# Performance work log

Measured on AMD Instinct MI355X. Metric: run time of the kernel, lower is better.

## Reference

```python
import jax, jax.numpy as jnp
import numpy as np

G = 8  # order of C8 rotation group

def expand_circulant(w):
    # w: [out_fields, in_fields, G] free params of a C8 regular->regular 1x1 conv.
    # Full weight: W[of*G+go, if*G+gi] = w[of, if, (go-gi) mod G]
    g = jnp.arange(G)
    idx = (g[:, None] - g[None, :]) % G            # [go, gi]
    Wf = w[:, :, idx]                              # [of, if, go, gi]
    Wf = jnp.transpose(Wf, (0, 2, 1, 3))           # [of, go, if, gi]
    return Wf.reshape(w.shape[0] * G, w.shape[1] * G)

def eq_proj(x2, w, b):
    # x2: [B, in_fields*G]; equivariant 1x1 conv = GEMM with circulant-expanded weight
    Wf = expand_circulant(w)                       # [out_fields*G, in_fields*G]
    bf = jnp.repeat(b, G)                          # per-field bias, shared across group dim
    return x2 @ Wf.T + bf

def setup_inputs() -> dict:
    key = jax.random.key(0)
    ks = jax.random.split(key, 12)
    B, d_model, n_head, d_k, d_v = 8192, 128, 8, 64, 64
    C = d_model * G                                # 1024
    s_in = 0.02
    inp = {
        'q': jax.random.normal(ks[0], (B, C, 1, 1), jnp.float32),
        'k': jax.random.normal(ks[1], (B, C, 1, 1), jnp.float32),
        'v': jax.random.normal(ks[2], (B, C, 1, 1), jnp.float32),
        'w_q': jax.random.normal(ks[3], (n_head * d_k, d_model, G), jnp.float32) * s_in,
        'b_q': jnp.zeros((n_head * d_k,), jnp.float32),
        'w_k': jax.random.normal(ks[4], (n_head * d_k, d_model, G), jnp.float32) * s_in,
        'b_k': jnp.zeros((n_head * d_k,), jnp.float32),
        'w_v': jax.random.normal(ks[5], (n_head * d_v, d_model, G), jnp.float32) * s_in,
        'b_v': jnp.zeros((n_head * d_v,), jnp.float32),
        'w_fc': jax.random.normal(ks[6], (d_model, n_head * d_v, G), jnp.float32) * s_in,
        'b_fc': jnp.zeros((d_model,), jnp.float32),
    }
    return inp

def reference(q, k, v, w_q, b_q, w_k, b_k, w_v, b_v, w_fc, b_fc):
    B, C = q.shape[0], q.shape[1]
    n_head, d_k = 8, 64
    d_v = 64
    temp = jnp.asarray(d_k ** 0.5, q.dtype)
    residual = q                                   # [B, C, 1, 1]
    q2 = q.reshape(B, C)
    k2 = k.reshape(B, C)
    v2 = v.reshape(B, C)
    # equivariant 1x1 conv projections -> [B, n_head*d_k*G]
    qp = eq_proj(q2, w_q, b_q).reshape(B, G, n_head, d_k).transpose(0, 2, 1, 3)  # [B,H,G,dk]
    kp = eq_proj(k2, w_k, b_k).reshape(B, G, n_head, d_k).transpose(0, 2, 1, 3)
    vp = eq_proj(v2, w_v, b_v).reshape(B, G, n_head, d_v).transpose(0, 2, 1, 3)
    # scaled dot-product attention over the G=8 group/orientation positions
    attn = jax.nn.softmax(jnp.einsum('bhqd,bhkd->bhqk', qp / temp, kp), axis=-1)  # [B,H,G,G]
    out = jnp.einsum('bhqk,bhkd->bhqd', attn, vp)  # [B,H,G,dv]
    # transpose(1,2) then flatten, exactly as torch .view(sz_b, -1, 1, 1)
    out = out.transpose(0, 2, 1, 3).reshape(B, G * n_head * d_v)
    out = eq_proj(out, w_fc, b_fc)                 # [B, d_model*G]
    out = out.reshape(B, C, 1, 1) + residual
    return out, attn
```

## Files before the change

### kernel.cpp

```cpp
#include <hip/hip_runtime.h>
#include <hip/hip_bf16.h>

typedef unsigned short u16;
typedef unsigned int u32;
typedef __bf16 bf16x8_t __attribute__((ext_vector_type(8)));
typedef float f32x4_t __attribute__((ext_vector_type(4)));

#define TILE 128
#define BK 64

__device__ __forceinline__ float b2f(u16 v) {
  return __uint_as_float(((u32)v) << 16);
}
__device__ __forceinline__ u16 f2b(float f) {
  __hip_bfloat16 h = __float2bfloat16(f);
  return *reinterpret_cast<u16*>(&h);
}
__device__ __forceinline__ float blo(u32 u) { return __uint_as_float(u << 16); }
__device__ __forceinline__ float bhi(u32 u) { return __uint_as_float(u & 0xffff0000u); }

__device__ __forceinline__ void async_lds16(const u16* g, u16* l) {
  __builtin_amdgcn_global_load_lds(
      (__attribute__((address_space(1))) void*)g,
      (__attribute__((address_space(3))) void*)l, 16, 0, 0);
}

__device__ __forceinline__ void cvt8(const float* __restrict__ src,
                                     u16* __restrict__ dst, size_t i) {
  float4 a = *(const float4*)(src + i);
  float4 b = *(const float4*)(src + i + 4);
  u16 t[8] = {f2b(a.x), f2b(a.y), f2b(a.z), f2b(a.w),
              f2b(b.x), f2b(b.y), f2b(b.z), f2b(b.w)};
  *(uint4*)(dst + i) = *(const uint4*)t;
}

__device__ __forceinline__ void expand8(const float* __restrict__ w,
                                        u16* __restrict__ dst, int I,
                                        int kshift, int gid) {
  const int n = gid >> kshift;
  const int kc = (gid & ((1 << kshift) - 1)) * 8;
  const int K = 8 << kshift;
  const float* wp = w + (size_t)((n >> 3) * I + (kc >> 3)) * 8;
  float4 w0 = *(const float4*)wp;
  float4 w1 = *(const float4*)(wp + 4);
  float w8[8] = {w0.x, w0.y, w0.z, w0.w, w1.x, w1.y, w1.z, w1.w};
  u16 t[8];
  const int r = (n - kc) & 7;
#pragma unroll
  for (int j = 0; j < 8; ++j) t[j] = f2b(w8[(r - j) & 7]);
  *(uint4*)(dst + (size_t)n * K + kc) = *(const uint4*)t;
}

__global__ __launch_bounds__(256) void prep_kernel(
    const float* __restrict__ q, const float* __restrict__ k,
    const float* __restrict__ v, u16* __restrict__ qb, u16* __restrict__ kb,
    u16* __restrict__ vb, const float* __restrict__ w_q,
    const float* __restrict__ w_k, const float* __restrict__ w_v,
    const float* __restrict__ w_fc, u16* __restrict__ Wq, u16* __restrict__ Wk,
    u16* __restrict__ Wv, u16* __restrict__ Wfc, int C) {
  const int bid = blockIdx.x;
  const int tid = threadIdx.x;
  if (bid < 3 * C) {
    const int plane = bid / C;
    const int b2 = bid - plane * C;
    const float* src = (plane == 0) ? q : (plane == 1) ? k : v;
    u16* dst = (plane == 0) ? qb : (plane == 1) ? kb : vb;
    cvt8(src, dst, ((size_t)b2 * 256 + tid) * 8);
  } else {
    const int e = bid - 3 * C;
    const int plane = e >> 11;
    const int gid = (e & 2047) * 256 + tid;
    if (plane == 0) expand8(w_q, Wq, 128, 7, gid);
    else if (plane == 1) expand8(w_k, Wk, 128, 7, gid);
    else if (plane == 2) expand8(w_v, Wv, 128, 7, gid);
    else expand8(w_fc, Wfc, 512, 9, gid);
  }
}

template <bool HAS_RES, bool OUT_F32>
__device__ __forceinline__ void gemm_core(
    const u16* __restrict__ X, const u16* __restrict__ W,
    const float* __restrict__ bias, const float* __restrict__ res,
    void* __restrict__ Yv, int M, int N, int K, int bid) {
  __shared__ __align__(16) u16 As[TILE * BK];
  __shared__ __align__(16) u16 Bs[TILE * BK];
  const int tid = threadIdx.x;

  const int grid_m = M >> 7, grid_n = N >> 7;
  const int nb = grid_m * grid_n;
  int pid = (bid & 7) * (nb >> 3) + (bid >> 3);
  const int nig = 8 * grid_n;
  const int group_id = pid / nig;
  const int first_m = group_id * 8;
  const int gsz = min(8, grid_m - first_m);
  const int mt = first_m + (pid % gsz);
  const int nt = (pid % nig) / gsz;
  const int m0 = mt << 7, n0 = nt << 7;

  const int lane = tid & 63;
  const int wave = tid >> 6;
  const int wm = (wave >> 1) * 64;
  const int wn = (wave & 1) * 64;
  const int l16 = lane & 15;
  const int quad = lane >> 4;

  f32x4_t acc[4][4] = {};

  const int row0 = tid >> 3;
  const int kgl = ((tid & 7) ^ (row0 & 7)) * 8;

  for (int k0 = 0; k0 < K; k0 += BK) {
#pragma unroll
    for (int it = 0; it < 4; ++it) {
      const int row = row0 + it * 32;
      const int off = (tid + it * 256) * 8;
      async_lds16(X + (size_t)(m0 + row) * K + (k0 + kgl), &As[off]);
      async_lds16(W + (size_t)(n0 + row) * K + (k0 + kgl), &Bs[off]);
    }
    __syncthreads();
#pragma unroll
    for (int half = 0; half < 2; ++half) {
      bf16x8_t af[4], bfr[4];
#pragma unroll
      for (int i = 0; i < 4; ++i)
        af[i] = *(const bf16x8_t*)&As[(wm + i * 16 + l16) * BK +
                                      (((quad + half * 4) ^ (l16 & 7)) * 8)];
#pragma unroll
      for (int j = 0; j < 4; ++j)
        bfr[j] = *(const bf16x8_t*)&Bs[(wn + j * 16 + l16) * BK +
                                       (((quad + half * 4) ^ (l16 & 7)) * 8)];
#pragma unroll
      for (int i = 0; i < 4; ++i)
#pragma unroll
        for (int j = 0; j < 4; ++j)
          acc[i][j] =
              __builtin_amdgcn_mfma_f32_16x16x32_bf16(af[i], bfr[j], acc[i][j], 0, 0, 0);
    }
    __syncthreads();
  }

#pragma unroll
  for (int j = 0; j < 4; ++j) {
    const int col = n0 + wn + j * 16 + l16;
    const float bv = bias[col >> 3];
#pragma unroll
    for (int i = 0; i < 4; ++i) {
#pragma unroll
      for (int r = 0; r < 4; ++r) {
        const int rw = m0 + wm + i * 16 + quad * 4 + r;
        float vv = acc[i][j][r] + bv;
        if (HAS_RES) vv += res[(size_t)rw * N + col];
        if (OUT_F32)
          ((float*)Yv)[(size_t)rw * N + col] = vv;
        else
          ((u16*)Yv)[(size_t)rw * N + col] = f2b(vv);
      }
    }
  }
}

__global__ __launch_bounds__(256) void gemm_qkv(
    const u16* __restrict__ X0, const u16* __restrict__ X1,
    const u16* __restrict__ X2, const u16* __restrict__ W0,
    const u16* __restrict__ W1, const u16* __restrict__ W2,
    const float* __restrict__ b0, const float* __restrict__ b1,
    const float* __restrict__ b2, u16* __restrict__ Y0, u16* __restrict__ Y1,
    u16* __restrict__ Y2, int M, int N, int K) {
  const int z = blockIdx.y;
  const u16* X = (z == 0) ? X0 : (z == 1) ? X1 : X2;
  const u16* W = (z == 0) ? W0 : (z == 1) ? W1 : W2;
  const float* bb = (z == 0) ? b0 : (z == 1) ? b1 : b2;
  u16* Y = (z == 0) ? Y0 : (z == 1) ? Y1 : Y2;
  gemm_core<false, false>(X, W, bb, nullptr, Y, M, N, K, blockIdx.x);
}

__global__ __launch_bounds__(256) void gemm_fc(
    const u16* __restrict__ X, const u16* __restrict__ W,
    const float* __restrict__ bias, const float* __restrict__ res,
    float* __restrict__ Y, int M, int N, int K) {
  gemm_core<true, true>(X, W, bias, res, Y, M, N, K, blockIdx.x);
}

__global__ __launch_bounds__(256) void attn_kernel(
    const u16* __restrict__ qp, const u16* __restrict__ kp,
    const u16* __restrict__ vp, float* __restrict__ probs,
    u16* __restrict__ o, int iters) {
  __shared__ __align__(16) u16 Qs[4][8 * 72];
  __shared__ __align__(16) u16 Ks[4][8 * 72];
  __shared__ __align__(16) u16 Vs[4][8 * 72];
  __shared__ float Ps[4][64];
  const int tid = threadIdx.x;
  const int wave = tid >> 6;
  const int lane = tid & 63;
  const int r = lane >> 3, c = lane & 7;
  const int ls = r * 72 + c * 8;
  const int qg = lane >> 3;
  const int kg = lane & 7;

  auto gaddr = [&](int it) {
    const int pair = (it * gridDim.x + blockIdx.x) * 4 + wave;
    return (size_t)(pair >> 3) * 4096 + (size_t)r * 512 + (pair & 7) * 64 + c * 8;
  };

  uint4 qr = *(const uint4*)(qp + gaddr(0));
  uint4 kr = *(const uint4*)(kp + gaddr(0));
  uint4 vr = *(const uint4*)(vp + gaddr(0));

  for (int it = 0; it < iters; ++it) {
    *(uint4*)&Qs[wave][ls] = qr;
    *(uint4*)&Ks[wave][ls] = kr;
    *(uint4*)&Vs[wave][ls] = vr;
    if (it + 1 < iters) {
      qr = *(const uint4*)(qp + gaddr(it + 1));
      kr = *(const uint4*)(kp + gaddr(it + 1));
      vr = *(const uint4*)(vp + gaddr(it + 1));
    }
    const int pair = (it * gridDim.x + blockIdx.x) * 4 + wave;
    const int b = pair >> 3;
    const int h = pair & 7;
    float s = 0.f;
#pragma unroll
    for (int d8 = 0; d8 < 8; ++d8) {
      uint4 qa = *(const uint4*)&Qs[wave][qg * 72 + d8 * 8];
      uint4 ka = *(const uint4*)&Ks[wave][kg * 72 + d8 * 8];
      s += blo(qa.x) * blo(ka.x) + bhi(qa.x) * bhi(ka.x);
      s += blo(qa.y) * blo(ka.y) + bhi(qa.y) * bhi(ka.y);
      s += blo(qa.z) * blo(ka.z) + bhi(qa.z) * bhi(ka.z);
      s += blo(qa.w) * blo(ka.w) + bhi(qa.w) * bhi(ka.w);
    }
    s *= 0.125f;
    float mx = s;
    mx = fmaxf(mx, __shfl_xor(mx, 1));
    mx = fmaxf(mx, __shfl_xor(mx, 2));
    mx = fmaxf(mx, __shfl_xor(mx, 4));
    float e = __expf(s - mx);
    float sum = e;
    sum += __shfl_xor(sum, 1);
    sum += __shfl_xor(sum, 2);
    sum += __shfl_xor(sum, 4);
    const float p = e / sum;
    probs[(size_t)pair * 64 + lane] = p;
    Ps[wave][lane] = p;
    float vc[8];
#pragma unroll
    for (int k2 = 0; k2 < 8; ++k2) vc[k2] = b2f(Vs[wave][k2 * 72 + lane]);
#pragma unroll
    for (int q2 = 0; q2 < 8; ++q2) {
      float acc = 0.f;
#pragma unroll
      for (int k2 = 0; k2 < 8; ++k2) acc += Ps[wave][q2 * 8 + k2] * vc[k2];
      o[(size_t)b * 4096 + q2 * 512 + h * 64 + lane] = f2b(acc);
    }
  }
}

extern "C" void kernel_launch(void* const* d_in, const int* in_sizes, int n_in,
                              void* d_out, int out_size, void* d_ws, size_t ws_size,
                              hipStream_t stream) {
  const float* q = (const float*)d_in[0];
  const float* k = (const float*)d_in[1];
  const float* v = (const float*)d_in[2];
  const float* w_q = (const float*)d_in[3];
  const float* b_q = (const float*)d_in[4];
  const float* w_k = (const float*)d_in[5];
  const float* b_k = (const float*)d_in[6];
  const float* w_v = (const float*)d_in[7];
  const float* b_v = (const float*)d_in[8];
  const float* w_fc = (const float*)d_in[9];
  const float* b_fc = (const float*)d_in[10];

  const int B = in_sizes[0] / 1024;
  float* out = (float*)d_out;
  float* probs = out + (size_t)B * 1024;

  u16* Wq = (u16*)d_ws;
  u16* Wk = Wq + (size_t)4096 * 1024;
  u16* Wv = Wk + (size_t)4096 * 1024;
  u16* Wfc = Wv + (size_t)4096 * 1024;
  u16* scratch = Wfc + (size_t)4096 * 1024;
  const size_t wbytes = (size_t)4 * 4096 * 1024 * sizeof(u16);

  const size_t per_row = (size_t)(3 * 1024 + 4 * 4096) * sizeof(u16);
  int chunkB = 128;
  for (int c = B; c >= 128; c >>= 1) {
    if (wbytes + (size_t)c * per_row <= ws_size) { chunkB = c; break; }
  }

  u16* qb = scratch;
  u16* kb = qb + (size_t)chunkB * 1024;
  u16* vb = kb + (size_t)chunkB * 1024;
  u16* qp = vb + (size_t)chunkB * 1024;
  u16* kp = qp + (size_t)chunkB * 4096;
  u16* vp = kp + (size_t)chunkB * 4096;
  u16* ao = vp + (size_t)chunkB * 4096;

  for (int cs = 0; cs < B; cs += chunkB) {
    const int C = chunkB / 2;
    const int prepBlocks = 3 * C + (cs == 0 ? 4 * 2048 : 0);
    prep_kernel<<<prepBlocks, 256, 0, stream>>>(
        q + (size_t)cs * 1024, k + (size_t)cs * 1024, v + (size_t)cs * 1024,
        qb, kb, vb, w_q, w_k, w_v, w_fc, Wq, Wk, Wv, Wfc, C);

    const int nb_p = (chunkB / TILE) * (4096 / TILE);
    gemm_qkv<<<dim3(nb_p, 3), 256, 0, stream>>>(qb, kb, vb, Wq, Wk, Wv, b_q,
                                                b_k, b_v, qp, kp, vp, chunkB,
                                                4096, 1024);
    const int ablocks = (chunkB >= 1024) ? 2048 : chunkB * 2;
    const int aiters = (chunkB * 8) / (ablocks * 4);
    attn_kernel<<<ablocks, 256, 0, stream>>>(qp, kp, vp,
                                             probs + (size_t)cs * 512, ao, aiters);
    const int nb_fc = (chunkB / TILE) * (1024 / TILE);
    gemm_fc<<<nb_fc, 256, 0, stream>>>(ao, Wfc, b_fc, q + (size_t)cs * 1024,
                                       out + (size_t)cs * 1024, chunkB, 1024,
                                       4096);
  }
}
```

Before: 658.9 us.

## Fuse fp32-to-bf16 input conversion into QKV GEMM and narrow FC tile

Drops the separate prep pass that wrote bf16 copies of q/k/v. The QKV GEMM now loads fp32 activations directly, converts them in registers and stores them to LDS, which removes a full extra read/write pass and the scratch buffers it used. Weight expansion moves to its own kernel, launched once. The FC GEMM uses 64-wide N tiles to get more blocks, and the attention kernel reads V straight from global instead of staging it in LDS. In exchange, A-tile loads become synchronous register loads rather than async LDS loads, which may expose more latency in the QKV GEMM.

```diff
diff --git a/kernel.cpp b/kernel.cpp
--- a/kernel.cpp
+++ b/kernel.cpp
@@ -6,7 +6,6 @@
 typedef __bf16 bf16x8_t __attribute__((ext_vector_type(8)));
 typedef float f32x4_t __attribute__((ext_vector_type(4)));
 
-#define TILE 128
 #define BK 64
 
 __device__ __forceinline__ float b2f(u16 v) {
@@ -23,15 +22,6 @@
   __builtin_amdgcn_global_load_lds(
       (__attribute__((address_space(1))) void*)g,
       (__attribute__((address_space(3))) void*)l, 16, 0, 0);
-}
-
-__device__ __forceinline__ void cvt8(const float* __restrict__ src,
-                                     u16* __restrict__ dst, size_t i) {
-  float4 a = *(const float4*)(src + i);
-  float4 b = *(const float4*)(src + i + 4);
-  u16 t[8] = {f2b(a.x), f2b(a.y), f2b(a.z), f2b(a.w),
-              f2b(b.x), f2b(b.y), f2b(b.z), f2b(b.w)};
-  *(uint4*)(dst + i) = *(const uint4*)t;
 }
 
 __device__ __forceinline__ void expand8(const float* __restrict__ w,
@@ -51,42 +41,30 @@
   *(uint4*)(dst + (size_t)n * K + kc) = *(const uint4*)t;
 }
 
-__global__ __launch_bounds__(256) void prep_kernel(
-    const float* __restrict__ q, const float* __restrict__ k,
-    const float* __restrict__ v, u16* __restrict__ qb, u16* __restrict__ kb,
-    u16* __restrict__ vb, const float* __restrict__ w_q,
-    const float* __restrict__ w_k, const float* __restrict__ w_v,
-    const float* __restrict__ w_fc, u16* __restrict__ Wq, u16* __restrict__ Wk,
-    u16* __restrict__ Wv, u16* __restrict__ Wfc, int C) {
-  const int bid = blockIdx.x;
-  const int tid = threadIdx.x;
-  if (bid < 3 * C) {
-    const int plane = bid / C;
-    const int b2 = bid - plane * C;
-    const float* src = (plane == 0) ? q : (plane == 1) ? k : v;
-    u16* dst = (plane == 0) ? qb : (plane == 1) ? kb : vb;
-    cvt8(src, dst, ((size_t)b2 * 256 + tid) * 8);
-  } else {
-    const int e = bid - 3 * C;
-    const int plane = e >> 11;
-    const int gid = (e & 2047) * 256 + tid;
-    if (plane == 0) expand8(w_q, Wq, 128, 7, gid);
-    else if (plane == 1) expand8(w_k, Wk, 128, 7, gid);
-    else if (plane == 2) expand8(w_v, Wv, 128, 7, gid);
-    else expand8(w_fc, Wfc, 512, 9, gid);
-  }
-}
-
-template <bool HAS_RES, bool OUT_F32>
+__global__ __launch_bounds__(256) void expand_all(
+    const float* __restrict__ w_q, const float* __restrict__ w_k,
+    const float* __restrict__ w_v, const float* __restrict__ w_fc,
+    u16* __restrict__ Wq, u16* __restrict__ Wk, u16* __restrict__ Wv,
+    u16* __restrict__ Wfc) {
+  const int e = blockIdx.x;
+  const int plane = e >> 11;
+  const int gid = (e & 2047) * 256 + threadIdx.x;
+  if (plane == 0) expand8(w_q, Wq, 128, 7, gid);
+  else if (plane == 1) expand8(w_k, Wk, 128, 7, gid);
+  else if (plane == 2) expand8(w_v, Wv, 128, 7, gid);
+  else expand8(w_fc, Wfc, 512, 9, gid);
+}
+
+template <int TN, bool HAS_RES, bool OUT_F32, bool A_F32>
 __device__ __forceinline__ void gemm_core(
-    const u16* __restrict__ X, const u16* __restrict__ W,
+    const void* __restrict__ Xv, const u16* __restrict__ W,
     const float* __restrict__ bias, const float* __restrict__ res,
     void* __restrict__ Yv, int M, int N, int K, int bid) {
-  __shared__ __align__(16) u16 As[TILE * BK];
-  __shared__ __align__(16) u16 Bs[TILE * BK];
+  __shared__ __align__(16) u16 As[128 * BK];
+  __shared__ __align__(16) u16 Bs[TN * BK];
   const int tid = threadIdx.x;
 
-  const int grid_m = M >> 7, grid_n = N >> 7;
+  const int grid_m = M >> 7, grid_n = N / TN;
   const int nb = grid_m * grid_n;
   int pid = (bid & 7) * (nb >> 3) + (bid >> 3);
   const int nig = 8 * grid_n;
@@ -95,44 +73,64 @@
   const int gsz = min(8, grid_m - first_m);
   const int mt = first_m + (pid % gsz);
   const int nt = (pid % nig) / gsz;
-  const int m0 = mt << 7, n0 = nt << 7;
+  const int m0 = mt << 7, n0 = nt * TN;
 
   const int lane = tid & 63;
   const int wave = tid >> 6;
   const int wm = (wave >> 1) * 64;
-  const int wn = (wave & 1) * 64;
+  const int wn = (wave & 1) * (TN / 2);
   const int l16 = lane & 15;
   const int quad = lane >> 4;
-
-  f32x4_t acc[4][4] = {};
+  constexpr int NJ = TN >> 5;
+
+  f32x4_t acc[4][NJ] = {};
 
   const int row0 = tid >> 3;
   const int kgl = ((tid & 7) ^ (row0 & 7)) * 8;
 
   for (int k0 = 0; k0 < K; k0 += BK) {
 #pragma unroll
-    for (int it = 0; it < 4; ++it) {
-      const int row = row0 + it * 32;
-      const int off = (tid + it * 256) * 8;
-      async_lds16(X + (size_t)(m0 + row) * K + (k0 + kgl), &As[off]);
-      async_lds16(W + (size_t)(n0 + row) * K + (k0 + kgl), &Bs[off]);
+    for (int it = 0; it < TN / 32; ++it)
+      async_lds16(W + (size_t)(n0 + row0 + it * 32) * K + (k0 + kgl),
+                  &Bs[(tid + it * 256) * 8]);
+    if (A_F32) {
+      const float* Xf = (const float*)Xv;
+      float4 fa[4], fb[4];
+#pragma unroll
+      for (int it = 0; it < 4; ++it) {
+        const float* p = Xf + (size_t)(m0 + row0 + it * 32) * K + (k0 + kgl);
+        fa[it] = *(const float4*)p;
+        fb[it] = *(const float4*)(p + 4);
+      }
+#pragma unroll
+      for (int it = 0; it < 4; ++it) {
+        u16 t[8] = {f2b(fa[it].x), f2b(fa[it].y), f2b(fa[it].z), f2b(fa[it].w),
+                    f2b(fb[it].x), f2b(fb[it].y), f2b(fb[it].z), f2b(fb[it].w)};
+        *(uint4*)&As[(tid + it * 256) * 8] = *(const uint4*)t;
+      }
+    } else {
+      const u16* Xb = (const u16*)Xv;
+#pragma unroll
+      for (int it = 0; it < 4; ++it)
+        async_lds16(Xb + (size_t)(m0 + row0 + it * 32) * K + (k0 + kgl),
+                    &As[(tid + it * 256) * 8]);
     }
     __syncthreads();
 #pragma unroll
     for (int half = 0; half < 2; ++half) {
-      bf16x8_t af[4], bfr[4];
+      bf16x8_t af[4], bfr[NJ];
 #pragma unroll
       for (int i = 0; i < 4; ++i)
         af[i] = *(const bf16x8_t*)&As[(wm + i * 16 + l16) * BK +
                                       (((quad + half * 4) ^ (l16 & 7)) * 8)];
 #pragma unroll
-      for (int j = 0; j < 4; ++j)
+      for (int j = 0; j < NJ; ++j)
         bfr[j] = *(const bf16x8_t*)&Bs[(wn + j * 16 + l16) * BK +
                                        (((quad + half * 4) ^ (l16 & 7)) * 8)];
 #pragma unroll
       for (int i = 0; i < 4; ++i)
 #pragma unroll
-        for (int j = 0; j < 4; ++j)
+        for (int j = 0; j < NJ; ++j)
           acc[i][j] =
               __builtin_amdgcn_mfma_f32_16x16x32_bf16(af[i], bfr[j], acc[i][j], 0, 0, 0);
     }
@@ -140,7 +138,7 @@
   }
 
 #pragma unroll
-  for (int j = 0; j < 4; ++j) {
+  for (int j = 0; j < NJ; ++j) {
     const int col = n0 + wn + j * 16 + l16;
     const float bv = bias[col >> 3];
 #pragma unroll
@@ -160,25 +158,25 @@
 }
 
 __global__ __launch_bounds__(256) void gemm_qkv(
-    const u16* __restrict__ X0, const u16* __restrict__ X1,
-    const u16* __restrict__ X2, const u16* __restrict__ W0,
+    const float* __restrict__ X0, const float* __restrict__ X1,
+    const float* __restrict__ X2, const u16* __restrict__ W0,
     const u16* __restrict__ W1, const u16* __restrict__ W2,
     const float* __restrict__ b0, const float* __restrict__ b1,
     const float* __restrict__ b2, u16* __restrict__ Y0, u16* __restrict__ Y1,
     u16* __restrict__ Y2, int M, int N, int K) {
   const int z = blockIdx.y;
-  const u16* X = (z == 0) ? X0 : (z == 1) ? X1 : X2;
+  const float* X = (z == 0) ? X0 : (z == 1) ? X1 : X2;
   const u16* W = (z == 0) ? W0 : (z == 1) ? W1 : W2;
   const float* bb = (z == 0) ? b0 : (z == 1) ? b1 : b2;
   u16* Y = (z == 0) ? Y0 : (z == 1) ? Y1 : Y2;
-  gemm_core<false, false>(X, W, bb, nullptr, Y, M, N, K, blockIdx.x);
+  gemm_core<128, false, false, true>(X, W, bb, nullptr, Y, M, N, K, blockIdx.x);
 }
 
 __global__ __launch_bounds__(256) void gemm_fc(
     const u16* __restrict__ X, const u16* __restrict__ W,
     const float* __restrict__ bias, const float* __restrict__ res,
     float* __restrict__ Y, int M, int N, int K) {
-  gemm_core<true, true>(X, W, bias, res, Y, M, N, K, blockIdx.x);
+  gemm_core<64, true, true, false>(X, W, bias, res, Y, M, N, K, blockIdx.x);
 }
 
 __global__ __launch_bounds__(256) void attn_kernel(
@@ -187,37 +185,38 @@
     u16* __restrict__ o, int iters) {
   __shared__ __align__(16) u16 Qs[4][8 * 72];
   __shared__ __align__(16) u16 Ks[4][8 * 72];
-  __shared__ __align__(16) u16 Vs[4][8 * 72];
-  __shared__ float Ps[4][64];
+  __shared__ __align__(16) float Ps[4][64];
   const int tid = threadIdx.x;
   const int wave = tid >> 6;
   const int lane = tid & 63;
   const int r = lane >> 3, c = lane & 7;
   const int ls = r * 72 + c * 8;
-  const int qg = lane >> 3;
-  const int kg = lane & 7;
-
+  const int qg = r;
+  const int kg = c;
+
+  auto pairof = [&](int it) { return (it * gridDim.x + blockIdx.x) * 4 + wave; };
   auto gaddr = [&](int it) {
-    const int pair = (it * gridDim.x + blockIdx.x) * 4 + wave;
-    return (size_t)(pair >> 3) * 4096 + (size_t)r * 512 + (pair & 7) * 64 + c * 8;
+    const int pr = pairof(it);
+    return (size_t)(pr >> 3) * 4096 + (size_t)r * 512 + (pr & 7) * 64 + c * 8;
   };
 
   uint4 qr = *(const uint4*)(qp + gaddr(0));
   uint4 kr = *(const uint4*)(kp + gaddr(0));
-  uint4 vr = *(const uint4*)(vp + gaddr(0));
 
   for (int it = 0; it < iters; ++it) {
     *(uint4*)&Qs[wave][ls] = qr;
     *(uint4*)&Ks[wave][ls] = kr;
-    *(uint4*)&Vs[wave][ls] = vr;
+    const int pair = pairof(it);
+    const int b = pair >> 3;
+    const int h = pair & 7;
+    float vcf[8];
+#pragma unroll
+    for (int k2 = 0; k2 < 8; ++k2)
+      vcf[k2] = b2f(vp[(size_t)b * 4096 + (size_t)k2 * 512 + h * 64 + lane]);
     if (it + 1 < iters) {
       qr = *(const uint4*)(qp + gaddr(it + 1));
       kr = *(const uint4*)(kp + gaddr(it + 1));
-      vr = *(const uint4*)(vp + gaddr(it + 1));
-    }
-    const int pair = (it * gridDim.x + blockIdx.x) * 4 + wave;
-    const int b = pair >> 3;
-    const int h = pair & 7;
+    }
     float s = 0.f;
 #pragma unroll
     for (int d8 = 0; d8 < 8; ++d8) {
@@ -241,14 +240,12 @@
     const float p = e / sum;
     probs[(size_t)pair * 64 + lane] = p;
     Ps[wave][lane] = p;
-    float vc[8];
-#pragma unroll
-    for (int k2 = 0; k2 < 8; ++k2) vc[k2] = b2f(Vs[wave][k2 * 72 + lane]);
 #pragma unroll
     for (int q2 = 0; q2 < 8; ++q2) {
-      float acc = 0.f;
-#pragma unroll
-      for (int k2 = 0; k2 < 8; ++k2) acc += Ps[wave][q2 * 8 + k2] * vc[k2];
+      float4 p0 = *(const float4*)&Ps[wave][q2 * 8];
+      float4 p1 = *(const float4*)&Ps[wave][q2 * 8 + 4];
+      float acc = p0.x * vcf[0] + p0.y * vcf[1] + p0.z * vcf[2] + p0.w * vcf[3] +
+                  p1.x * vcf[4] + p1.y * vcf[5] + p1.z * vcf[6] + p1.w * vcf[7];
       o[(size_t)b * 4096 + q2 * 512 + h * 64 + lane] = f2b(acc);
     }
   }
@@ -280,36 +277,29 @@
   u16* scratch = Wfc + (size_t)4096 * 1024;
   const size_t wbytes = (size_t)4 * 4096 * 1024 * sizeof(u16);
 
-  const size_t per_row = (size_t)(3 * 1024 + 4 * 4096) * sizeof(u16);
+  const size_t per_row = (size_t)(4 * 4096) * sizeof(u16);
   int chunkB = 128;
   for (int c = B; c >= 128; c >>= 1) {
     if (wbytes + (size_t)c * per_row <= ws_size) { chunkB = c; break; }
   }
 
-  u16* qb = scratch;
-  u16* kb = qb + (size_t)chunkB * 1024;
-  u16* vb = kb + (size_t)chunkB * 1024;
-  u16* qp = vb + (size_t)chunkB * 1024;
+  u16* qp = scratch;
   u16* kp = qp + (size_t)chunkB * 4096;
   u16* vp = kp + (size_t)chunkB * 4096;
   u16* ao = vp + (size_t)chunkB * 4096;
 
+  expand_all<<<8192, 256, 0, stream>>>(w_q, w_k, w_v, w_fc, Wq, Wk, Wv, Wfc);
+
   for (int cs = 0; cs < B; cs += chunkB) {
-    const int C = chunkB / 2;
-    const int prepBlocks = 3 * C + (cs == 0 ? 4 * 2048 : 0);
-    prep_kernel<<<prepBlocks, 256, 0, stream>>>(
+    const int nb_p = (chunkB / 128) * (4096 / 128);
+    gemm_qkv<<<dim3(nb_p, 3), 256, 0, stream>>>(
         q + (size_t)cs * 1024, k + (size_t)cs * 1024, v + (size_t)cs * 1024,
-        qb, kb, vb, w_q, w_k, w_v, w_fc, Wq, Wk, Wv, Wfc, C);
-
-    const int nb_p = (chunkB / TILE) * (4096 / TILE);
-    gemm_qkv<<<dim3(nb_p, 3), 256, 0, stream>>>(qb, kb, vb, Wq, Wk, Wv, b_q,
-                                                b_k, b_v, qp, kp, vp, chunkB,
-                                                4096, 1024);
+        Wq, Wk, Wv, b_q, b_k, b_v, qp, kp, vp, chunkB, 4096, 1024);
     const int ablocks = (chunkB >= 1024) ? 2048 : chunkB * 2;
     const int aiters = (chunkB * 8) / (ablocks * 4);
     attn_kernel<<<ablocks, 256, 0, stream>>>(qp, kp, vp,
                                              probs + (size_t)cs * 512, ao, aiters);
-    const int nb_fc = (chunkB / TILE) * (1024 / TILE);
+    const int nb_fc = (chunkB / 128) * (1024 / 64);
     gemm_fc<<<nb_fc, 256, 0, stream>>>(ao, Wfc, b_fc, q + (size_t)cs * 1024,
                                        out + (size_t)cs * 1024, chunkB, 1024,
                                        4096);
```

Measured after the change: 605.5 us. -8.1%, faster.
